# Kernel tuning notes

Measured on AMD Instinct MI355X. Metric: run time of the kernel, lower is better.

Reference implementation:

```python
import jax, jax.numpy as jnp
import numpy as np

B, S, D = 2, 2048, 768
NH, GH = 12, 4
HD = D // NH            # 64
GD = HD * GH            # 256 (grouped KV projection width)
REP = NH // GH          # 3  (repeat factor for KV heads)
SCALE = HD ** -0.5
MASK_FILL = -1e-09      # faithful to the original (NOT -1e9)


def setup_inputs() -> dict:
    key = jax.random.key(0)
    ks = jax.random.split(key, 9)
    init = 0.02
    x = jax.random.normal(ks[0], (B, S, D), dtype=jnp.float32)
    masks = jnp.tril(jnp.ones((S, S), dtype=jnp.float32)) > 0  # bool causal mask
    Wq = jax.random.normal(ks[1], (D, D), dtype=jnp.float32) * init
    bq = jnp.zeros((D,), dtype=jnp.float32)
    Wk = jax.random.normal(ks[2], (D, GD), dtype=jnp.float32) * init
    bk = jnp.zeros((GD,), dtype=jnp.float32)
    Wv = jax.random.normal(ks[3], (D, GD), dtype=jnp.float32) * init
    bv = jnp.zeros((GD,), dtype=jnp.float32)
    Wo = jax.random.normal(ks[4], (D, D), dtype=jnp.float32) * init
    bo = jnp.zeros((D,), dtype=jnp.float32)
    return {"x": x, "masks": masks, "Wq": Wq, "bq": bq, "Wk": Wk, "bk": bk,
            "Wv": Wv, "bv": bv, "Wo": Wo, "bo": bo}


def reference(x, masks, Wq, bq, Wk, bk, Wv, bv, Wo, bo):
    bs, seq, _ = x.shape
    # projections (weights stored [in, out])
    q = (x @ Wq + bq).reshape(bs, seq, NH, HD).transpose(0, 2, 1, 3)   # [b, nh, s, hd]
    k = (x @ Wk + bk).reshape(bs, seq, GH, HD).transpose(0, 2, 1, 3)   # [b, gh, s, hd]
    v = (x @ Wv + bv).reshape(bs, seq, GH, HD).transpose(0, 2, 1, 3)
    # repeat_interleave KV heads to match query heads (faithful to original)
    k = jnp.repeat(k, REP, axis=1)                                     # [b, nh, s, hd]
    v = jnp.repeat(v, REP, axis=1)
    scores = jnp.einsum('bhqd,bhkd->bhqk', q, k) * SCALE               # [b, nh, s, s]
    # original: masked_fill(masks == 0, -1e-09)
    scores = jnp.where(masks, scores, MASK_FILL)
    attn = jax.nn.softmax(scores, axis=-1)
    out = jnp.einsum('bhqk,bhkd->bhqd', attn, v)                       # [b, nh, s, hd]
    # faithful to original buggy merge: transpose(-1,-2).contiguous().view(b, s, dim)
    out = out.transpose(0, 1, 3, 2).reshape(bs, seq, D)
    return out @ Wo + bo
```

## Files before the change

kernel.cpp:

```cpp
#include <hip/hip_runtime.h>
#include <stdint.h>


typedef unsigned short ushort_t;
typedef short bf16x8 __attribute__((ext_vector_type(8)));
typedef float f32x4 __attribute__((ext_vector_type(4)));

#define MFMA(a, b, c) __builtin_amdgcn_mfma_f32_16x16x32_bf16((a), (b), (c), 0, 0, 0)

__device__ __forceinline__ ushort_t f2bf(float f) {
    union { float f; unsigned u; } v; v.f = f;
    const unsigned r = v.u + 0x7FFFu + ((v.u >> 16) & 1u);
    return (ushort_t)(r >> 16);
}

__global__ __launch_bounds__(256) void prep_x(const float* __restrict__ x,
                                              ushort_t* __restrict__ xb) {
    const int i = (blockIdx.x * 256 + threadIdx.x) * 4;
    const float4 v = *(const float4*)(x + i);
    uint2 p;
    p.x = (unsigned)f2bf(v.x) | ((unsigned)f2bf(v.y) << 16);
    p.y = (unsigned)f2bf(v.z) | ((unsigned)f2bf(v.w) << 16);
    *(uint2*)(xb + i) = p;
}

__global__ __launch_bounds__(256) void prep_w(
    const float* __restrict__ Wq, const float* __restrict__ Wk,
    const float* __restrict__ Wv, const float* __restrict__ Wo,
    ushort_t* __restrict__ WqT, ushort_t* __restrict__ WkT,
    ushort_t* __restrict__ WvT, ushort_t* __restrict__ WoT) {
    const int z = blockIdx.z;
    const float* src; ushort_t* dst; int N;
    if (z == 0)      { src = Wq; dst = WqT; N = 768; }
    else if (z == 1) { src = Wk; dst = WkT; N = 256; }
    else if (z == 2) { src = Wv; dst = WvT; N = 256; }
    else             { src = Wo; dst = WoT; N = 768; }
    const int k0 = blockIdx.x * 64, n0 = blockIdx.y * 64;
    if (n0 >= N) return;

    __shared__ float Ts[64][65];
    const int tid = threadIdx.x;
    const int r = tid >> 2, cb = (tid & 3) * 16;
    #pragma unroll
    for (int jj = 0; jj < 4; ++jj) {
        const float4 v = *(const float4*)(src + (k0 + r) * N + n0 + cb + jj * 4);
        Ts[cb + jj * 4 + 0][r] = v.x; Ts[cb + jj * 4 + 1][r] = v.y;
        Ts[cb + jj * 4 + 2][r] = v.z; Ts[cb + jj * 4 + 3][r] = v.w;
    }
    __syncthreads();
    const int n = tid >> 2, kc = (tid & 3) * 16;
    unsigned hbuf[16];
    #pragma unroll
    for (int j = 0; j < 16; ++j) hbuf[j] = f2bf(Ts[n][kc + j]);
    uint4 p0, p1;
    p0.x = hbuf[0] | (hbuf[1] << 16);   p0.y = hbuf[2] | (hbuf[3] << 16);
    p0.z = hbuf[4] | (hbuf[5] << 16);   p0.w = hbuf[6] | (hbuf[7] << 16);
    p1.x = hbuf[8] | (hbuf[9] << 16);   p1.y = hbuf[10] | (hbuf[11] << 16);
    p1.z = hbuf[12] | (hbuf[13] << 16); p1.w = hbuf[14] | (hbuf[15] << 16);
    *(uint4*)(dst + (n0 + n) * 768 + k0 + kc) = p0;
    *(uint4*)(dst + (n0 + n) * 768 + k0 + kc + 8) = p1;
}

__global__ __launch_bounds__(256) void qkv_kernel(
    const ushort_t* __restrict__ xb,
    const ushort_t* __restrict__ WqT, const ushort_t* __restrict__ WkT,
    const ushort_t* __restrict__ WvT,
    const float* __restrict__ bq, const float* __restrict__ bk,
    const float* __restrict__ bv,
    ushort_t* __restrict__ Qb, ushort_t* __restrict__ Kb,
    ushort_t* __restrict__ Vtb) {
    const int ct = blockIdx.x, rt = blockIdx.y;
    const int r0 = rt * 64;
    const ushort_t* WT; const float* bias; int head; int kind;
    if (ct < 12)      { WT = WqT; bias = bq; head = ct;      kind = 0; }
    else if (ct < 16) { WT = WkT; bias = bk; head = ct - 12; kind = 1; }
    else              { WT = WvT; bias = bv; head = ct - 16; kind = 2; }
    const int n0 = head * 64;

    __shared__ uint4 Xs[512];
    __shared__ uint4 Ws[512];

    const int tid = threadIdx.x;
    const int lane = tid & 63, w = tid >> 6;
    const int quad = lane >> 4, l15 = lane & 15;
    const int sr = tid >> 2, sb = (tid & 3) * 2;

    f32x4 acc[4] = {{0,0,0,0},{0,0,0,0},{0,0,0,0},{0,0,0,0}};

    for (int k0 = 0; k0 < 768; k0 += 64) {
        __syncthreads();
        #pragma unroll
        for (int c = 0; c < 2; ++c) {
            const int blk = sb + c;
            Xs[sr * 8 + (blk ^ (sr & 7))] = *(const uint4*)(xb + (r0 + sr) * 768 + k0 + blk * 8);
            Ws[sr * 8 + (blk ^ (sr & 7))] = *(const uint4*)(WT + (n0 + sr) * 768 + k0 + blk * 8);
        }
        __syncthreads();
        #pragma unroll
        for (int ks = 0; ks < 2; ++ks) {
            const int arow = 16 * w + l15;
            const bf16x8 af = *(const bf16x8*)&Xs[arow * 8 + ((quad + 4 * ks) ^ (arow & 7))];
            #pragma unroll
            for (int ctt = 0; ctt < 4; ++ctt) {
                const int brow = 16 * ctt + l15;
                const bf16x8 bfr = *(const bf16x8*)&Ws[brow * 8 + ((quad + 4 * ks) ^ (brow & 7))];
                acc[ctt] = MFMA(af, bfr, acc[ctt]);
            }
        }
    }
    #pragma unroll
    for (int ctt = 0; ctt < 4; ++ctt) {
        const int cd = ctt * 16 + l15;
        const float bv_ = bias[n0 + cd];
        const int row0 = r0 + 16 * w + quad * 4;
        const int b = row0 >> 11;
        if (kind == 2) {
            const int s0 = row0 & 2047;
            unsigned h[4];
            #pragma unroll
            for (int reg = 0; reg < 4; ++reg) h[reg] = f2bf(acc[ctt][reg] + bv_);
            uint2 pk; pk.x = h[0] | (h[1] << 16); pk.y = h[2] | (h[3] << 16);
            *(uint2*)(Vtb + ((b * 4 + head) * 64 + cd) * 2048 + s0) = pk;
        } else {
            #pragma unroll
            for (int reg = 0; reg < 4; ++reg) {
                const int row = row0 + reg;
                const int s = row & 2047;
                const float pre = acc[ctt][reg] + bv_;
                const ushort_t hh = f2bf((kind == 0) ? pre * 0.125f : pre);
                if (kind == 0) Qb[((b * 12 + head) * 2048 + s) * 64 + cd] = hh;
                else           Kb[((b * 4 + head) * 2048 + s) * 64 + cd] = hh;
            }
        }
    }
}

__global__ __launch_bounds__(256) void v_suffix_kernel(
    const ushort_t* __restrict__ Vtb, float* __restrict__ SV) {
    const int b = blockIdx.z, g = blockIdx.y, d0 = blockIdx.x * 8;
    const int tid = threadIdx.x;
    const int dd = tid >> 5, tt = tid & 31;
    const ushort_t* vp = Vtb + ((b * 4 + g) * 64 + d0 + dd) * 2048 + tt * 64;
    float s = 0.f;
    #pragma unroll
    for (int j = 0; j < 8; ++j) {
        const bf16x8 v = *(const bf16x8*)(vp + j * 8);
        #pragma unroll
        for (int e = 0; e < 8; ++e) {
            union { unsigned u; float f; } c;
            c.u = ((unsigned)(ushort_t)v[e]) << 16;
            s += c.f;
        }
    }
    __shared__ float cs[8][32];
    cs[dd][tt] = s;
    __syncthreads();
    if (tid < 8) {
        float run = 0.f;
        const int base = ((b * 4 + g) * 32) * 64 + d0 + tid;
        for (int j = 31; j >= 0; --j) {
            run += cs[tid][j];
            SV[base + j * 64] = run;
        }
    }
}

__global__ __launch_bounds__(256) void attn_kernel(
    const ushort_t* __restrict__ Qb, const ushort_t* __restrict__ Kb,
    const ushort_t* __restrict__ Vtb, const float* __restrict__ SV,
    ushort_t* __restrict__ aT_hi, ushort_t* __restrict__ aT_lo) {
    const int qt = 31 - (int)blockIdx.x;
    const int h = blockIdx.y, b = blockIdx.z;
    const int g = h / 3;
    const int q0 = qt * 64;
    const int tid = threadIdx.x;
    const int lane = tid & 63, w = tid >> 6;
    const int quad = lane >> 4, l15 = lane & 15;

    __shared__ uint4 K_l[512];
    __shared__ uint4 V_l[512];
    __shared__ __align__(16) ushort_t P_l[64 * 72];

    const ushort_t* Qp = Qb + ((b * 12 + h) * 2048 + q0 + 16 * w + l15) * 64;
    const bf16x8 qf0 = *(const bf16x8*)(Qp + quad * 8);
    const bf16x8 qf1 = *(const bf16x8*)(Qp + 32 + quad * 8);

    const ushort_t* Kp = Kb + (b * 4 + g) * 2048 * 64;
    const ushort_t* Vp = Vtb + (b * 4 + g) * 64 * 2048;

    f32x4 o[4] = {{0,0,0,0},{0,0,0,0},{0,0,0,0},{0,0,0,0}};
    float lacc[4] = {0.f, 0.f, 0.f, 0.f};

    const int sr = tid >> 2, sb = (tid & 3) * 2;
    const int qg = q0 + 16 * w + quad * 4;
    const int prow = (16 * w + quad * 4) * 72;

    auto stage_kv = [&](int k0) {
        #pragma unroll
        for (int c = 0; c < 2; ++c) {
            const int blk = sb + c;
            K_l[sr * 8 + (blk ^ (sr & 7))] = *(const uint4*)(Kp + (k0 + sr) * 64 + blk * 8);
            V_l[sr * 8 + (blk ^ (sr & 7))] = *(const uint4*)(Vp + sr * 2048 + k0 + blk * 8);
        }
    };
    auto do_pv = [&]() {
        const bf16x8 pf0 = *(const bf16x8*)&P_l[(16 * w + l15) * 72 + quad * 8];
        const bf16x8 pf1 = *(const bf16x8*)&P_l[(16 * w + l15) * 72 + 32 + quad * 8];
        #pragma unroll
        for (int ctt = 0; ctt < 4; ++ctt) {
            const int d = ctt * 16 + l15;
            o[ctt] = MFMA(pf0, *(const bf16x8*)&V_l[d * 8 + ((quad + 0) ^ (d & 7))], o[ctt]);
            o[ctt] = MFMA(pf1, *(const bf16x8*)&V_l[d * 8 + ((quad + 4) ^ (d & 7))], o[ctt]);
        }
    };

    for (int k0 = 0; k0 < q0; k0 += 64) {
        __syncthreads();
        stage_kv(k0);
        __syncthreads();
        #pragma unroll
        for (int ctt = 0; ctt < 4; ++ctt) {
            const int key = ctt * 16 + l15;
            f32x4 s = {0, 0, 0, 0};
            s = MFMA(qf0, *(const bf16x8*)&K_l[key * 8 + ((quad + 0) ^ (key & 7))], s);
            s = MFMA(qf1, *(const bf16x8*)&K_l[key * 8 + ((quad + 4) ^ (key & 7))], s);
            #pragma unroll
            for (int reg = 0; reg < 4; ++reg) {
                const float e = __expf(s[reg]);
                lacc[reg] += e;
                P_l[prow + reg * 72 + key] = f2bf(e);
            }
        }
        do_pv();
    }

    {
        __syncthreads();
        stage_kv(q0);
        __syncthreads();
        #pragma unroll
        for (int ctt = 0; ctt < 4; ++ctt) {
            const int key = ctt * 16 + l15;
            f32x4 s = {0, 0, 0, 0};
            s = MFMA(qf0, *(const bf16x8*)&K_l[key * 8 + ((quad + 0) ^ (key & 7))], s);
            s = MFMA(qf1, *(const bf16x8*)&K_l[key * 8 + ((quad + 4) ^ (key & 7))], s);
            const int kg = q0 + key;
            #pragma unroll
            for (int reg = 0; reg < 4; ++reg) {
                float e = __expf(s[reg]);
                e = (kg <= qg + reg) ? e : 1.0f;
                lacc[reg] += e;
                P_l[prow + reg * 72 + key] = f2bf(e);
            }
        }
        do_pv();
    }

    if (qt < 31) {
        const float* svp = SV + ((b * 4 + g) * 32 + qt + 1) * 64;
        #pragma unroll
        for (int ctt = 0; ctt < 4; ++ctt) {
            const float t = svp[ctt * 16 + l15];
            #pragma unroll
            for (int reg = 0; reg < 4; ++reg) o[ctt][reg] += t;
        }
    }
    const float tailc = (float)(2048 - 64 - q0);

    #pragma unroll
    for (int reg = 0; reg < 4; ++reg) {
        float v = lacc[reg];
        v += __shfl_xor(v, 1); v += __shfl_xor(v, 2);
        v += __shfl_xor(v, 4); v += __shfl_xor(v, 8);
        lacc[reg] = 1.f / (v + tailc);
    }
    const int t0 = q0 + 16 * w + quad * 4;
    #pragma unroll
    for (int ctt = 0; ctt < 4; ++ctt) {
        const int d = ctt * 16 + l15;
        unsigned hh[4], hl[4];
        #pragma unroll
        for (int reg = 0; reg < 4; ++reg) {
            const float val = o[ctt][reg] * lacc[reg];
            const ushort_t hi = f2bf(val);
            union { unsigned u; float f; } vv; vv.u = (unsigned)hi << 16;
            hh[reg] = hi;
            hl[reg] = f2bf(val - vv.f);
        }
        const int idx = (b * 768 + h * 64 + d) * 2048 + t0;
        uint2 ph, pl;
        ph.x = hh[0] | (hh[1] << 16); ph.y = hh[2] | (hh[3] << 16);
        pl.x = hl[0] | (hl[1] << 16); pl.y = hl[2] | (hl[3] << 16);
        *(uint2*)(aT_hi + idx) = ph;
        *(uint2*)(aT_lo + idx) = pl;
    }
}

__global__ __launch_bounds__(256) void out_proj_kernel(
    const ushort_t* __restrict__ aT_hi, const ushort_t* __restrict__ aT_lo,
    const ushort_t* __restrict__ WoT, const float* __restrict__ bo,
    float* __restrict__ out) {
    const int ct = blockIdx.x, rt = blockIdx.y;
    const int r0 = rt * 64, c0 = ct * 64;
    __shared__ uint4 Ah[512];
    __shared__ uint4 Al[512];
    __shared__ uint4 Ws[512];
    const int tid = threadIdx.x;
    const int lane = tid & 63, w = tid >> 6;
    const int quad = lane >> 4, l15 = lane & 15;
    const int sr = tid >> 2, sb = (tid & 3) * 2;

    f32x4 acc[4] = {{0,0,0,0},{0,0,0,0},{0,0,0,0},{0,0,0,0}};

    for (int k0 = 0; k0 < 768; k0 += 64) {
        __syncthreads();
        #pragma unroll
        for (int c = 0; c < 2; ++c) {
            const int blk = sb + c;
            const int slot = sr * 8 + (blk ^ (sr & 7));
            Ah[slot] = *(const uint4*)(aT_hi + (r0 + sr) * 768 + k0 + blk * 8);
            Al[slot] = *(const uint4*)(aT_lo + (r0 + sr) * 768 + k0 + blk * 8);
            Ws[slot] = *(const uint4*)(WoT + (c0 + sr) * 768 + k0 + blk * 8);
        }
        __syncthreads();
        #pragma unroll
        for (int ks = 0; ks < 2; ++ks) {
            const int arow = 16 * w + l15;
            const int aslot = arow * 8 + ((quad + 4 * ks) ^ (arow & 7));
            const bf16x8 ah = *(const bf16x8*)&Ah[aslot];
            const bf16x8 al = *(const bf16x8*)&Al[aslot];
            #pragma unroll
            for (int ctt = 0; ctt < 4; ++ctt) {
                const int brow = 16 * ctt + l15;
                const bf16x8 bfr = *(const bf16x8*)&Ws[brow * 8 + ((quad + 4 * ks) ^ (brow & 7))];
                acc[ctt] = MFMA(ah, bfr, acc[ctt]);
                acc[ctt] = MFMA(al, bfr, acc[ctt]);
            }
        }
    }
    #pragma unroll
    for (int ctt = 0; ctt < 4; ++ctt) {
        const int cd = c0 + ctt * 16 + l15;
        const float bo_v = bo[cd];
        #pragma unroll
        for (int reg = 0; reg < 4; ++reg) {
            const int row = r0 + 16 * w + quad * 4 + reg;
            out[row * 768 + cd] = acc[ctt][reg] + bo_v;
        }
    }
}

extern "C" void kernel_launch(void* const* d_in, const int* in_sizes, int n_in,
                              void* d_out, int out_size, void* d_ws, size_t ws_size,
                              hipStream_t stream) {
    const float* x  = (const float*)d_in[0];
    const float* Wq = (const float*)d_in[2];
    const float* bq = (const float*)d_in[3];
    const float* Wk = (const float*)d_in[4];
    const float* bk = (const float*)d_in[5];
    const float* Wv = (const float*)d_in[6];
    const float* bv = (const float*)d_in[7];
    const float* Wo = (const float*)d_in[8];
    const float* bo = (const float*)d_in[9];
    float* out = (float*)d_out;

    uint8_t* wsb = (uint8_t*)d_ws;
    ushort_t* xb    = (ushort_t*)(wsb);
    ushort_t* WqT   = (ushort_t*)(wsb + 6291456);
    ushort_t* WkT   = (ushort_t*)(wsb + 7471104);
    ushort_t* WvT   = (ushort_t*)(wsb + 7864320);
    ushort_t* WoT   = (ushort_t*)(wsb + 8257536);
    ushort_t* Qb    = (ushort_t*)(wsb + 9437184);
    ushort_t* Kb    = (ushort_t*)(wsb + 15728640);
    ushort_t* Vtb   = (ushort_t*)(wsb + 17825792);
    ushort_t* aT_hi = (ushort_t*)(wsb + 19922944);
    ushort_t* aT_lo = (ushort_t*)(wsb + 26214400);
    float* SV = (float*)wsb;

    prep_x<<<3072, 256, 0, stream>>>(x, xb);
    prep_w<<<dim3(12, 12, 4), 256, 0, stream>>>(Wq, Wk, Wv, Wo, WqT, WkT, WvT, WoT);
    qkv_kernel<<<dim3(20, 64), 256, 0, stream>>>(xb, WqT, WkT, WvT, bq, bk, bv, Qb, Kb, Vtb);
    v_suffix_kernel<<<dim3(8, 4, 2), 256, 0, stream>>>(Vtb, SV);
    attn_kernel<<<dim3(32, 12, 2), 256, 0, stream>>>(Qb, Kb, Vtb, SV, aT_hi, aT_lo);
    out_proj_kernel<<<dim3(12, 64), 256, 0, stream>>>(aT_hi, aT_lo, WoT, bo, out);
}
```

Measured before the change: 200.7 us.

## Double-buffer K/V tiles in attention and dispatch heavy query tiles first

The attention kernel now prefetches the next K/V tile into registers while computing on the current one, writing it into a second LDS buffer. This cuts the per-iteration barriers from two to one and hides global load latency behind the MFMA work. The grid is also reordered so that all heads and batches of the longest causal query tiles launch first, which should improve load balance across CUs. In exchange it doubles the K/V LDS footprint and adds register pressure from the prefetch buffers, which could lower occupancy.

Measured after the change: 201.0 us. About the same (+0.1%).

```diff
diff --git a/kernel.cpp b/kernel.cpp
--- a/kernel.cpp
+++ b/kernel.cpp
@@ -169,16 +169,18 @@
     const ushort_t* __restrict__ Qb, const ushort_t* __restrict__ Kb,
     const ushort_t* __restrict__ Vtb, const float* __restrict__ SV,
     ushort_t* __restrict__ aT_hi, ushort_t* __restrict__ aT_lo) {
-    const int qt = 31 - (int)blockIdx.x;
-    const int h = blockIdx.y, b = blockIdx.z;
+    const int hb = blockIdx.x;
+    const int h = hb % 12, b = hb / 12;
+    const int qt = 31 - (int)blockIdx.y;
     const int g = h / 3;
     const int q0 = qt * 64;
+    const int nt = qt + 1;
     const int tid = threadIdx.x;
     const int lane = tid & 63, w = tid >> 6;
     const int quad = lane >> 4, l15 = lane & 15;
 
-    __shared__ uint4 K_l[512];
-    __shared__ uint4 V_l[512];
+    __shared__ uint4 K_l[2][512];
+    __shared__ uint4 V_l[2][512];
     __shared__ __align__(16) ushort_t P_l[64 * 72];
 
     const ushort_t* Qp = Qb + ((b * 12 + h) * 2048 + q0 + 16 * w + l15) * 64;
@@ -195,65 +197,71 @@
     const int qg = q0 + 16 * w + quad * 4;
     const int prow = (16 * w + quad * 4) * 72;
 
-    auto stage_kv = [&](int k0) {
+    uint4 rK[2], rV[2];
+    auto issue_loads = [&](int t) {
+        const int k0 = t * 64;
         #pragma unroll
         for (int c = 0; c < 2; ++c) {
             const int blk = sb + c;
-            K_l[sr * 8 + (blk ^ (sr & 7))] = *(const uint4*)(Kp + (k0 + sr) * 64 + blk * 8);
-            V_l[sr * 8 + (blk ^ (sr & 7))] = *(const uint4*)(Vp + sr * 2048 + k0 + blk * 8);
+            rK[c] = *(const uint4*)(Kp + (k0 + sr) * 64 + blk * 8);
+            rV[c] = *(const uint4*)(Vp + sr * 2048 + k0 + blk * 8);
         }
     };
-    auto do_pv = [&]() {
-        const bf16x8 pf0 = *(const bf16x8*)&P_l[(16 * w + l15) * 72 + quad * 8];
-        const bf16x8 pf1 = *(const bf16x8*)&P_l[(16 * w + l15) * 72 + 32 + quad * 8];
-        #pragma unroll
-        for (int ctt = 0; ctt < 4; ++ctt) {
-            const int d = ctt * 16 + l15;
-            o[ctt] = MFMA(pf0, *(const bf16x8*)&V_l[d * 8 + ((quad + 0) ^ (d & 7))], o[ctt]);
-            o[ctt] = MFMA(pf1, *(const bf16x8*)&V_l[d * 8 + ((quad + 4) ^ (d & 7))], o[ctt]);
+    auto write_lds = [&](int buf) {
+        #pragma unroll
+        for (int c = 0; c < 2; ++c) {
+            const int blk = sb + c;
+            K_l[buf][sr * 8 + (blk ^ (sr & 7))] = rK[c];
+            V_l[buf][sr * 8 + (blk ^ (sr & 7))] = rV[c];
         }
     };
-
-    for (int k0 = 0; k0 < q0; k0 += 64) {
-        __syncthreads();
-        stage_kv(k0);
-        __syncthreads();
+    auto compute = [&](int t, int buf, bool diag) {
+        const int k0 = t * 64;
         #pragma unroll
         for (int ctt = 0; ctt < 4; ++ctt) {
             const int key = ctt * 16 + l15;
             f32x4 s = {0, 0, 0, 0};
-            s = MFMA(qf0, *(const bf16x8*)&K_l[key * 8 + ((quad + 0) ^ (key & 7))], s);
-            s = MFMA(qf1, *(const bf16x8*)&K_l[key * 8 + ((quad + 4) ^ (key & 7))], s);
-            #pragma unroll
-            for (int reg = 0; reg < 4; ++reg) {
-                const float e = __expf(s[reg]);
-                lacc[reg] += e;
-                P_l[prow + reg * 72 + key] = f2bf(e);
+            s = MFMA(qf0, *(const bf16x8*)&K_l[buf][key * 8 + ((quad + 0) ^ (key & 7))], s);
+            s = MFMA(qf1, *(const bf16x8*)&K_l[buf][key * 8 + ((quad + 4) ^ (key & 7))], s);
+            if (diag) {
+                const int kg = k0 + key;
+                #pragma unroll
+                for (int reg = 0; reg < 4; ++reg) {
+                    float e = __expf(s[reg]);
+                    e = (kg <= qg + reg) ? e : 1.0f;
+                    lacc[reg] += e;
+                    P_l[prow + reg * 72 + key] = f2bf(e);
+                }
+            } else {
+                #pragma unroll
+                for (int reg = 0; reg < 4; ++reg) {
+                    const float e = __expf(s[reg]);
+                    lacc[reg] += e;
+                    P_l[prow + reg * 72 + key] = f2bf(e);
+                }
             }
         }
-        do_pv();
-    }
-
-    {
-        __syncthreads();
-        stage_kv(q0);
-        __syncthreads();
+        const bf16x8 pf0 = *(const bf16x8*)&P_l[(16 * w + l15) * 72 + quad * 8];
+        const bf16x8 pf1 = *(const bf16x8*)&P_l[(16 * w + l15) * 72 + 32 + quad * 8];
         #pragma unroll
         for (int ctt = 0; ctt < 4; ++ctt) {
-            const int key = ctt * 16 + l15;
-            f32x4 s = {0, 0, 0, 0};
-            s = MFMA(qf0, *(const bf16x8*)&K_l[key * 8 + ((quad + 0) ^ (key & 7))], s);
-            s = MFMA(qf1, *(const bf16x8*)&K_l[key * 8 + ((quad + 4) ^ (key & 7))], s);
-            const int kg = q0 + key;
-            #pragma unroll
-            for (int reg = 0; reg < 4; ++reg) {
-                float e = __expf(s[reg]);
-                e = (kg <= qg + reg) ? e : 1.0f;
-                lacc[reg] += e;
-                P_l[prow + reg * 72 + key] = f2bf(e);
-            }
-        }
-        do_pv();
+            const int d = ctt * 16 + l15;
+            o[ctt] = MFMA(pf0, *(const bf16x8*)&V_l[buf][d * 8 + ((quad + 0) ^ (d & 7))], o[ctt]);
+            o[ctt] = MFMA(pf1, *(const bf16x8*)&V_l[buf][d * 8 + ((quad + 4) ^ (d & 7))], o[ctt]);
+        }
+    };
+
+    issue_loads(0);
+    write_lds(0);
+    if (nt > 1) issue_loads(1);
+    __syncthreads();
+    for (int t = 0; t < nt; ++t) {
+        if (t + 1 < nt) {
+            write_lds((t + 1) & 1);
+            if (t + 2 < nt) issue_loads(t + 2);
+        }
+        compute(t, t & 1, t == nt - 1);
+        __syncthreads();
     }
 
     if (qt < 31) {
@@ -381,6 +389,6 @@
     prep_w<<<dim3(12, 12, 4), 256, 0, stream>>>(Wq, Wk, Wv, Wo, WqT, WkT, WvT, WoT);
     qkv_kernel<<<dim3(20, 64), 256, 0, stream>>>(xb, WqT, WkT, WvT, bq, bk, bv, Qb, Kb, Vtb);
     v_suffix_kernel<<<dim3(8, 4, 2), 256, 0, stream>>>(Vtb, SV);
-    attn_kernel<<<dim3(32, 12, 2), 256, 0, stream>>>(Qb, Kb, Vtb, SV, aT_hi, aT_lo);
+    attn_kernel<<<dim3(24, 32), 256, 0, stream>>>(Qb, Kb, Vtb, SV, aT_hi, aT_lo);
     out_proj_kernel<<<dim3(12, 64), 256, 0, stream>>>(aT_hi, aT_lo, WoT, bo, out);
 }
```
